# Performance work log

Hardware: AMD Instinct MI355X
Metric: run time of the kernel (lower is better)

Reference implementation:

```python
import jax, jax.numpy as jnp
import numpy as np
from jax import lax

SEQ, BATCH, FEAT = 64, 32768, 15
H1 = H2 = H3 = 4  # hidden sizes from the source module


def setup_inputs() -> dict:
    key = jax.random.key(0)
    ks = jax.random.split(key, 11)
    s = 0.1
    return {
        "x": jax.random.normal(ks[0], (SEQ, BATCH, FEAT), jnp.float32),
        "w1": jax.random.normal(ks[1], (H1, FEAT), jnp.float32) * s,
        "b1": jax.random.normal(ks[2], (H1,), jnp.float32) * s,
        "w2": jax.random.normal(ks[3], (H2, H1), jnp.float32) * s,
        "b2": jax.random.normal(ks[4], (H2,), jnp.float32) * s,
        "w_ih": jax.random.normal(ks[5], (4 * H3, H2), jnp.float32) * s,
        "w_hh": jax.random.normal(ks[6], (4 * H3, H3), jnp.float32) * s,
        "b_ih": jax.random.normal(ks[7], (4 * H3,), jnp.float32) * s,
        "b_hh": jax.random.normal(ks[8], (4 * H3,), jnp.float32) * s,
        "w3": jax.random.normal(ks[9], (1, H3), jnp.float32) * s,
        "b3": jax.random.normal(ks[10], (1,), jnp.float32) * s,
    }


def reference(x, w1, b1, w2, b2, w_ih, w_hh, b_ih, b_hh, w3, b3):
    seq, batch, _ = x.shape
    hidden = w_hh.shape[1]
    # front-end MLP: fc1 -> relu -> fc2 -> sigmoid   (applied per timestep)
    h1 = jax.nn.relu(jnp.einsum('sbf,hf->sbh', x, w1) + b1)          # [S,B,H1]
    h2 = jax.nn.sigmoid(jnp.einsum('sbh,gh->sbg', h1, w2) + b2)      # [S,B,H2]
    # precompute input-to-gate projections for all timesteps: [S,B,4H]
    gx = jnp.einsum('sbh,gh->sbg', h2, w_ih) + b_ih + b_hh

    def step(carry, gxt):
        h, c = carry
        gates = gxt + h @ w_hh.T                                      # [B,4H]
        i, f, g, o = jnp.split(gates, 4, axis=-1)                     # torch order i,f,g,o
        i = jax.nn.sigmoid(i)
        f = jax.nn.sigmoid(f)
        g = jnp.tanh(g)
        o = jax.nn.sigmoid(o)
        c = f * c + i * g
        h = o * jnp.tanh(c)
        return (h, c), None

    h0 = jnp.zeros((batch, hidden), x.dtype)
    c0 = jnp.zeros((batch, hidden), x.dtype)
    (h_last, _), _ = lax.scan(step, (h0, c0), gx)                     # last-step hidden [B,H3]
    out = jax.nn.sigmoid(h_last @ w3.T + b3)                          # [B,1]
    return out.reshape(batch)
```

## Files before the change

kernel.cpp:

```cpp
#include <hip/hip_runtime.h>

#define SEQ   64
#define BATCH 32768
#define FEAT  15
#define SLAB  (BATCH * FEAT)

__device__ __forceinline__ float fast_rcp(float x) { return __builtin_amdgcn_rcpf(x); }

__device__ __forceinline__ float fast_sigmoid(float x) {
    return fast_rcp(1.0f + __expf(-x));
}
__device__ __forceinline__ float fast_tanh(float x) {
    return 1.0f - 2.0f * fast_rcp(1.0f + __expf(2.0f * x));
}

template <int CTRL>
__device__ __forceinline__ float qmov(float v) {
    return __int_as_float(
        __builtin_amdgcn_mov_dpp(__float_as_int(v), CTRL, 0xf, 0xf, false));
}

struct __attribute__((aligned(4))) F4 { float a, b, c, d; };
__device__ __forceinline__ F4 ldf4(const float* p) { return *(const F4*)p; }

__global__ __launch_bounds__(256, 2) void lstm_fused(
    const float* __restrict__ x,
    const float* __restrict__ w1,  const float* __restrict__ b1,
    const float* __restrict__ w2,  const float* __restrict__ b2,
    const float* __restrict__ wih, const float* __restrict__ whh,
    const float* __restrict__ bih, const float* __restrict__ bhh,
    const float* __restrict__ w3,  const float* __restrict__ b3,
    float* __restrict__ out)
{
    const int tid = threadIdx.x;
    const int w   = tid >> 6;
    const int l   = tid & 63;
    const int u   = l & 3;
    const int e   = l >> 2;
    const int ewave = blockIdx.x * 64 + w * 16;
    const int elem  = ewave + e;

    const int qoff = (u == 3) ? 11 : 4 * u;
    const float* xp = x + (size_t)elem * FEAT + qoff;

    float W1[FEAT], W2[4], WI[16], WH[16], BI[4];
#pragma unroll
    for (int f = 0; f < FEAT; ++f) W1[f] = w1[u * FEAT + f];
    const float B1v = b1[u];
#pragma unroll
    for (int j = 0; j < 4; ++j) W2[j] = w2[u * 4 + j];
    const float B2v = b2[u];
#pragma unroll
    for (int g = 0; g < 4; ++g) {
#pragma unroll
        for (int j = 0; j < 4; ++j) {
            WI[g * 4 + j] = wih[(g * 4 + u) * 4 + j];
            WH[g * 4 + j] = whh[(g * 4 + u) * 4 + j];
        }
        BI[g] = bih[g * 4 + u] + bhh[g * 4 + u];
    }
    const float W3v = w3[u];
    const float B3v = b3[0];

    float h = 0.0f, c = 0.0f;

    auto step = [&](F4 q) {
        float xv[FEAT];
        xv[0]  = qmov<0x00>(q.a); xv[1]  = qmov<0x00>(q.b);
        xv[2]  = qmov<0x00>(q.c); xv[3]  = qmov<0x00>(q.d);
        xv[4]  = qmov<0x55>(q.a); xv[5]  = qmov<0x55>(q.b);
        xv[6]  = qmov<0x55>(q.c); xv[7]  = qmov<0x55>(q.d);
        xv[8]  = qmov<0xAA>(q.a); xv[9]  = qmov<0xAA>(q.b);
        xv[10] = qmov<0xAA>(q.c); xv[11] = qmov<0xAA>(q.d);
        xv[12] = qmov<0xFF>(q.b); xv[13] = qmov<0xFF>(q.c);
        xv[14] = qmov<0xFF>(q.d);
        float a0 = B1v, a1 = 0.0f, a2 = 0.0f;
#pragma unroll
        for (int f = 0; f < 5; ++f) a0 = fmaf(W1[f],      xv[f],      a0);
#pragma unroll
        for (int f = 0; f < 5; ++f) a1 = fmaf(W1[5 + f],  xv[5 + f],  a1);
#pragma unroll
        for (int f = 0; f < 5; ++f) a2 = fmaf(W1[10 + f], xv[10 + f], a2);
        const float h1 = fmaxf(a0 + (a1 + a2), 0.0f);
        float q0 = qmov<0x00>(h1), q1 = qmov<0x55>(h1), q2 = qmov<0xAA>(h1), q3 = qmov<0xFF>(h1);
        const float a2f = B2v + W2[0] * q0 + W2[1] * q1 + W2[2] * q2 + W2[3] * q3;
        const float h2 = fast_sigmoid(a2f);
        q0 = qmov<0x00>(h2); q1 = qmov<0x55>(h2); q2 = qmov<0xAA>(h2); q3 = qmov<0xFF>(h2);
        float gi = BI[0] + WI[0]  * q0 + WI[1]  * q1 + WI[2]  * q2 + WI[3]  * q3;
        float gf = BI[1] + WI[4]  * q0 + WI[5]  * q1 + WI[6]  * q2 + WI[7]  * q3;
        float gg = BI[2] + WI[8]  * q0 + WI[9]  * q1 + WI[10] * q2 + WI[11] * q3;
        float go = BI[3] + WI[12] * q0 + WI[13] * q1 + WI[14] * q2 + WI[15] * q3;
        q0 = qmov<0x00>(h); q1 = qmov<0x55>(h); q2 = qmov<0xAA>(h); q3 = qmov<0xFF>(h);
        gi += WH[0]  * q0 + WH[1]  * q1 + WH[2]  * q2 + WH[3]  * q3;
        gf += WH[4]  * q0 + WH[5]  * q1 + WH[6]  * q2 + WH[7]  * q3;
        gg += WH[8]  * q0 + WH[9]  * q1 + WH[10] * q2 + WH[11] * q3;
        go += WH[12] * q0 + WH[13] * q1 + WH[14] * q2 + WH[15] * q3;
        const float ig = fast_sigmoid(gi);
        const float fg = fast_sigmoid(gf);
        const float gt = fast_tanh(gg);
        const float og = fast_sigmoid(go);
        c = fmaf(fg, c, ig * gt);
        h = og * fast_tanh(c);
    };

    F4 Q[8];
#pragma unroll
    for (int j = 0; j < 8; ++j) Q[j] = ldf4(xp + (size_t)j * SLAB);

#pragma unroll 1
    for (int i = 0; i < 7; ++i) {
        const float* xs = xp + (size_t)(8 * i + 8) * SLAB;
#pragma unroll
        for (int j = 0; j < 8; ++j) {
            F4 qcur = Q[j];
            Q[j] = ldf4(xs + (size_t)j * SLAB);
            step(qcur);
        }
    }
#pragma unroll
    for (int j = 0; j < 8; ++j) step(Q[j]);

    float p = W3v * h;
    p += qmov<0xB1>(p);
    p += qmov<0x4E>(p);
    if (u == 0) out[elem] = fast_sigmoid(p + B3v);
}

extern "C" void kernel_launch(void* const* d_in, const int* in_sizes, int n_in,
                              void* d_out, int out_size, void* d_ws, size_t ws_size,
                              hipStream_t stream) {
    (void)in_sizes; (void)n_in; (void)d_ws; (void)ws_size; (void)out_size;
    const float* x   = (const float*)d_in[0];
    const float* w1  = (const float*)d_in[1];
    const float* b1  = (const float*)d_in[2];
    const float* w2  = (const float*)d_in[3];
    const float* b2  = (const float*)d_in[4];
    const float* wih = (const float*)d_in[5];
    const float* whh = (const float*)d_in[6];
    const float* bih = (const float*)d_in[7];
    const float* bhh = (const float*)d_in[8];
    const float* w3  = (const float*)d_in[9];
    const float* b3  = (const float*)d_in[10];
    float* out = (float*)d_out;

    lstm_fused<<<dim3(512), dim3(256), 0, stream>>>(
        x, w1, b1, w2, b2, wih, whh, bih, bhh, w3, b3, out);
}
```

Before: 36.17 us.

## Fold log2e into weights and double-buffer x prefetch with sched barriers

Pre-scales the weights and biases by -log2e (and by 2·log2e for the tanh gate) so each activation uses a raw exp2 plus reciprocal, with no multiply before the exponential. The gate dot products become explicit fma chains. The loop now uses two register buffers of 8 timesteps each: the next 8 slabs are loaded while the current 8 are computed, and sched_barriers stop the compiler from interleaving the loads with the compute. This roughly doubles the live registers used for prefetched data, which could put pressure on the launch bound of 2 blocks per SIMD.

```diff
diff --git a/kernel.cpp b/kernel.cpp
--- a/kernel.cpp
+++ b/kernel.cpp
@@ -5,14 +5,10 @@
 #define FEAT  15
 #define SLAB  (BATCH * FEAT)
 
-__device__ __forceinline__ float fast_rcp(float x) { return __builtin_amdgcn_rcpf(x); }
+#define LOG2E 1.4426950408889634f
 
-__device__ __forceinline__ float fast_sigmoid(float x) {
-    return fast_rcp(1.0f + __expf(-x));
-}
-__device__ __forceinline__ float fast_tanh(float x) {
-    return 1.0f - 2.0f * fast_rcp(1.0f + __expf(2.0f * x));
-}
+__device__ __forceinline__ float fast_rcp(float x)  { return __builtin_amdgcn_rcpf(x); }
+__device__ __forceinline__ float ex2(float x)       { return __builtin_amdgcn_exp2f(x); }
 
 template <int CTRL>
 __device__ __forceinline__ float qmov(float v) {
@@ -37,8 +33,7 @@
     const int l   = tid & 63;
     const int u   = l & 3;
     const int e   = l >> 2;
-    const int ewave = blockIdx.x * 64 + w * 16;
-    const int elem  = ewave + e;
+    const int elem = blockIdx.x * 64 + w * 16 + e;
 
     const int qoff = (u == 3) ? 11 : 4 * u;
     const float* xp = x + (size_t)elem * FEAT + qoff;
@@ -48,19 +43,20 @@
     for (int f = 0; f < FEAT; ++f) W1[f] = w1[u * FEAT + f];
     const float B1v = b1[u];
 #pragma unroll
-    for (int j = 0; j < 4; ++j) W2[j] = w2[u * 4 + j];
-    const float B2v = b2[u];
+    for (int j = 0; j < 4; ++j) W2[j] = -LOG2E * w2[u * 4 + j];
+    const float B2v = -LOG2E * b2[u];
 #pragma unroll
     for (int g = 0; g < 4; ++g) {
+        const float sg = (g == 2) ? (2.0f * LOG2E) : -LOG2E;
 #pragma unroll
         for (int j = 0; j < 4; ++j) {
-            WI[g * 4 + j] = wih[(g * 4 + u) * 4 + j];
-            WH[g * 4 + j] = whh[(g * 4 + u) * 4 + j];
+            WI[g * 4 + j] = sg * wih[(g * 4 + u) * 4 + j];
+            WH[g * 4 + j] = sg * whh[(g * 4 + u) * 4 + j];
         }
-        BI[g] = bih[g * 4 + u] + bhh[g * 4 + u];
+        BI[g] = sg * (bih[g * 4 + u] + bhh[g * 4 + u]);
     }
-    const float W3v = w3[u];
-    const float B3v = b3[0];
+    const float W3v = -LOG2E * w3[u];
+    const float B3v = -LOG2E * b3[0];
 
     float h = 0.0f, c = 0.0f;
 
@@ -83,47 +79,57 @@
         for (int f = 0; f < 5; ++f) a2 = fmaf(W1[10 + f], xv[10 + f], a2);
         const float h1 = fmaxf(a0 + (a1 + a2), 0.0f);
         float q0 = qmov<0x00>(h1), q1 = qmov<0x55>(h1), q2 = qmov<0xAA>(h1), q3 = qmov<0xFF>(h1);
-        const float a2f = B2v + W2[0] * q0 + W2[1] * q1 + W2[2] * q2 + W2[3] * q3;
-        const float h2 = fast_sigmoid(a2f);
+        const float a2n = fmaf(W2[0], q0, fmaf(W2[1], q1, fmaf(W2[2], q2, fmaf(W2[3], q3, B2v))));
+        const float h2 = fast_rcp(1.0f + ex2(a2n));
         q0 = qmov<0x00>(h2); q1 = qmov<0x55>(h2); q2 = qmov<0xAA>(h2); q3 = qmov<0xFF>(h2);
-        float gi = BI[0] + WI[0]  * q0 + WI[1]  * q1 + WI[2]  * q2 + WI[3]  * q3;
-        float gf = BI[1] + WI[4]  * q0 + WI[5]  * q1 + WI[6]  * q2 + WI[7]  * q3;
-        float gg = BI[2] + WI[8]  * q0 + WI[9]  * q1 + WI[10] * q2 + WI[11] * q3;
-        float go = BI[3] + WI[12] * q0 + WI[13] * q1 + WI[14] * q2 + WI[15] * q3;
+        float gi = fmaf(WI[0],  q0, fmaf(WI[1],  q1, fmaf(WI[2],  q2, fmaf(WI[3],  q3, BI[0]))));
+        float gf = fmaf(WI[4],  q0, fmaf(WI[5],  q1, fmaf(WI[6],  q2, fmaf(WI[7],  q3, BI[1]))));
+        float gg = fmaf(WI[8],  q0, fmaf(WI[9],  q1, fmaf(WI[10], q2, fmaf(WI[11], q3, BI[2]))));
+        float go = fmaf(WI[12], q0, fmaf(WI[13], q1, fmaf(WI[14], q2, fmaf(WI[15], q3, BI[3]))));
         q0 = qmov<0x00>(h); q1 = qmov<0x55>(h); q2 = qmov<0xAA>(h); q3 = qmov<0xFF>(h);
-        gi += WH[0]  * q0 + WH[1]  * q1 + WH[2]  * q2 + WH[3]  * q3;
-        gf += WH[4]  * q0 + WH[5]  * q1 + WH[6]  * q2 + WH[7]  * q3;
-        gg += WH[8]  * q0 + WH[9]  * q1 + WH[10] * q2 + WH[11] * q3;
-        go += WH[12] * q0 + WH[13] * q1 + WH[14] * q2 + WH[15] * q3;
-        const float ig = fast_sigmoid(gi);
-        const float fg = fast_sigmoid(gf);
-        const float gt = fast_tanh(gg);
-        const float og = fast_sigmoid(go);
+        gi = fmaf(WH[0],  q0, fmaf(WH[1],  q1, fmaf(WH[2],  q2, fmaf(WH[3],  q3, gi))));
+        gf = fmaf(WH[4],  q0, fmaf(WH[5],  q1, fmaf(WH[6],  q2, fmaf(WH[7],  q3, gf))));
+        gg = fmaf(WH[8],  q0, fmaf(WH[9],  q1, fmaf(WH[10], q2, fmaf(WH[11], q3, gg))));
+        go = fmaf(WH[12], q0, fmaf(WH[13], q1, fmaf(WH[14], q2, fmaf(WH[15], q3, go))));
+        const float ig = fast_rcp(1.0f + ex2(gi));
+        const float fg = fast_rcp(1.0f + ex2(gf));
+        const float og = fast_rcp(1.0f + ex2(go));
+        const float gt = fmaf(-2.0f, fast_rcp(1.0f + ex2(gg)), 1.0f);
         c = fmaf(fg, c, ig * gt);
-        h = og * fast_tanh(c);
+        const float tc = fmaf(-2.0f, fast_rcp(1.0f + ex2(c * (2.0f * LOG2E))), 1.0f);
+        h = og * tc;
     };
 
-    F4 Q[8];
+    F4 Qa[8], Qb[8];
+    auto prefetch8 = [&](F4* Q, const float* base) {
 #pragma unroll
-    for (int j = 0; j < 8; ++j) Q[j] = ldf4(xp + (size_t)j * SLAB);
+        for (int j = 0; j < 8; ++j) Q[j] = ldf4(base + (size_t)j * SLAB);
+    };
+    auto compute8 = [&](F4* Q) {
+#pragma unroll
+        for (int j = 0; j < 8; ++j) step(Q[j]);
+    };
 
+    prefetch8(Qa, xp);
 #pragma unroll 1
-    for (int i = 0; i < 7; ++i) {
-        const float* xs = xp + (size_t)(8 * i + 8) * SLAB;
-#pragma unroll
-        for (int j = 0; j < 8; ++j) {
-            F4 qcur = Q[j];
-            Q[j] = ldf4(xs + (size_t)j * SLAB);
-            step(qcur);
-        }
+    for (int i = 0; i < 3; ++i) {
+        const float* bft = xp + (size_t)(16 * i + 8) * SLAB;
+        prefetch8(Qb, bft);
+        __builtin_amdgcn_sched_barrier(0);
+        compute8(Qa);
+        prefetch8(Qa, bft + (size_t)8 * SLAB);
+        __builtin_amdgcn_sched_barrier(0);
+        compute8(Qb);
     }
-#pragma unroll
-    for (int j = 0; j < 8; ++j) step(Q[j]);
+    prefetch8(Qb, xp + (size_t)56 * SLAB);
+    __builtin_amdgcn_sched_barrier(0);
+    compute8(Qa);
+    compute8(Qb);
 
     float p = W3v * h;
     p += qmov<0xB1>(p);
     p += qmov<0x4E>(p);
-    if (u == 0) out[elem] = fast_sigmoid(p + B3v);
+    if (u == 0) out[elem] = fast_rcp(1.0f + ex2(p + B3v));
 }
 
 extern "C" void kernel_launch(void* const* d_in, const int* in_sizes, int n_in,
```

Measured after the change: 35.46 us. 1.02x faster.
